# Optimization experiments

Measured on AMD Instinct MI355X. Metric: run time of the kernel, lower is better.

## Reference

```python
import jax, jax.numpy as jnp
import numpy as np

D = 1024
HEADS = 16
HEAD_DIM = D // HEADS
EPS = 1e-5


def layer_norm(x, gamma, beta):
    mu = jnp.mean(x, axis=-1, keepdims=True)
    var = jnp.mean(jnp.square(x - mu), axis=-1, keepdims=True)
    return (x - mu) * jax.lax.rsqrt(var + EPS) * gamma + beta


def setup_inputs() -> dict:
    key = jax.random.key(0)
    ks = jax.random.split(key, 8)
    B, S = 4, 2048
    s_in = 1.0 / np.sqrt(D)
    s_ffn = 1.0 / np.sqrt(4 * D)
    return {
        "x": jax.random.normal(ks[0], (B, S, D), dtype=jnp.float32),
        "ln1_g": jnp.ones((D,), jnp.float32),
        "ln1_b": jnp.zeros((D,), jnp.float32),
        "w_qkv": jax.random.uniform(ks[1], (D, 3 * D), jnp.float32, -s_in, s_in),
        "b_qkv": jnp.zeros((3 * D,), jnp.float32),
        "w_out": jax.random.uniform(ks[2], (D, D), jnp.float32, -s_in, s_in),
        "b_out": jnp.zeros((D,), jnp.float32),
        "ln2_g": jnp.ones((D,), jnp.float32),
        "ln2_b": jnp.zeros((D,), jnp.float32),
        "w_ffn1": jax.random.uniform(ks[3], (D, 4 * D), jnp.float32, -s_in, s_in),
        "b_ffn1": jnp.zeros((4 * D,), jnp.float32),
        "w_ffn2": jax.random.uniform(ks[4], (4 * D, D), jnp.float32, -s_ffn, s_ffn),
        "b_ffn2": jnp.zeros((D,), jnp.float32),
    }


def reference(x, ln1_g, ln1_b, w_qkv, b_qkv, w_out, b_out,
              ln2_g, ln2_b, w_ffn1, b_ffn1, w_ffn2, b_ffn2):
    B, S, Dm = x.shape
    h = layer_norm(x, ln1_g, ln1_b)
    qkv = h @ w_qkv + b_qkv  # [B,S,3D]
    q, k, v = jnp.split(qkv, 3, axis=-1)
    # [B,S,D] -> [B,H,S,hd]
    def to_heads(t):
        return t.reshape(B, S, HEADS, HEAD_DIM).transpose(0, 2, 1, 3)
    q, k, v = to_heads(q), to_heads(k), to_heads(v)
    scores = jnp.einsum('bhqd,bhkd->bhqk', q, k) / np.sqrt(HEAD_DIM).astype(np.float32)
    attn = jax.nn.softmax(scores, axis=-1)
    out = jnp.einsum('bhqk,bhkd->bhqd', attn, v)
    out = out.transpose(0, 2, 1, 3).reshape(B, S, Dm)
    x = x + (out @ w_out + b_out)
    h = layer_norm(x, ln2_g, ln2_b)
    h = jax.nn.gelu(h @ w_ffn1 + b_ffn1, approximate=False) @ w_ffn2 + b_ffn2
    return x + h
```

## Files before the change

### kernel.cpp

```cpp
#include <hip/hip_runtime.h>
#include <cstdint>
#include <cstddef>

typedef unsigned short u16;
typedef unsigned int   u32;
typedef __bf16 bf16x8 __attribute__((ext_vector_type(8)));
typedef float  f32x4  __attribute__((ext_vector_type(4)));
static_assert(sizeof(bf16x8) == 16, "bf16x8 must be 16B");
static_assert(sizeof(f32x4) == 16, "f32x4 must be 16B");

#define DEVI static __device__ __forceinline__

#define QSCALE 0.18033688011112042f

DEVI u16 f2bf(float x) {
  u32 u = __builtin_bit_cast(u32, x);
  u = (u + 0x7FFFu + ((u >> 16) & 1u)) >> 16;
  return (u16)u;
}

DEVI void gload16(const u16* g, u16* l) {
  __builtin_amdgcn_global_load_lds(
      (const __attribute__((address_space(1))) void*)g,
      (__attribute__((address_space(3))) void*)l, 16, 0, 0);
}

#define S_BARRIER() asm volatile("s_barrier" ::: "memory")
#define VMCNT(n) asm volatile("s_waitcnt vmcnt(" #n ")" ::: "memory")

template <int MO, int NACC>
DEVI void mm16(f32x4 (&acc)[NACC][4], const bf16x8 (&af)[4], const bf16x8 (&bf)[4]) {
  __builtin_amdgcn_s_setprio(1);
#pragma unroll
  for (int m = 0; m < 4; m++)
#pragma unroll
    for (int n = 0; n < 4; n++)
      acc[MO + m][n] =
          __builtin_amdgcn_mfma_f32_16x16x32_bf16(af[m], bf[n], acc[MO + m][n], 0, 0, 0);
  __builtin_amdgcn_s_setprio(0);
}

__global__ __launch_bounds__(256) void transpose_cvt(const float* __restrict__ W,
                                                     u16* __restrict__ WT,
                                                     int K, int N,
                                                     float scale, int nscale) {
  __shared__ float tile[32][33];
  int tx = threadIdx.x & 31, ty = threadIdx.x >> 5;
  int c0 = blockIdx.x * 32, r0 = blockIdx.y * 32;
#pragma unroll
  for (int i = 0; i < 4; i++)
    tile[ty + i * 8][tx] = W[(size_t)(r0 + ty + i * 8) * N + c0 + tx];
  __syncthreads();
#pragma unroll
  for (int i = 0; i < 4; i++) {
    int r = ty + i * 8;
    int n = c0 + r;
    float scl = (n < nscale) ? scale : 1.f;
    WT[(size_t)n * K + r0 + tx] = f2bf(tile[tx][r] * scl);
  }
}

__global__ __launch_bounds__(256) void prep_bias(const float* __restrict__ b,
                                                 float* __restrict__ o) {
  int i = blockIdx.x * 256 + threadIdx.x;
  o[i] = b[i] * (i < 1024 ? QSCALE : 1.f);
}

__global__ __launch_bounds__(256) void ln_k(const float* __restrict__ X,
                                            const float* __restrict__ gam,
                                            const float* __restrict__ bet,
                                            u16* __restrict__ H) {
  __shared__ float2 part[4];
  int row = blockIdx.x, t = threadIdx.x;
  const float4* xr = (const float4*)(X + (size_t)row * 1024);
  float4 v = xr[t];
  float s = v.x + v.y + v.z + v.w;
  float q = v.x * v.x + v.y * v.y + v.z * v.z + v.w * v.w;
#pragma unroll
  for (int o = 32; o > 0; o >>= 1) {
    s += __shfl_xor(s, o);
    q += __shfl_xor(q, o);
  }
  if ((t & 63) == 0) part[t >> 6] = make_float2(s, q);
  __syncthreads();
  float S = part[0].x + part[1].x + part[2].x + part[3].x;
  float Q = part[0].y + part[1].y + part[2].y + part[3].y;
  float mu = S * (1.f / 1024.f);
  float rs = rsqrtf(Q * (1.f / 1024.f) - mu * mu + 1e-5f);
  float4 gv = ((const float4*)gam)[t];
  float4 bv = ((const float4*)bet)[t];
  ushort4 o;
  o.x = f2bf((v.x - mu) * rs * gv.x + bv.x);
  o.y = f2bf((v.y - mu) * rs * gv.y + bv.y);
  o.z = f2bf((v.z - mu) * rs * gv.z + bv.z);
  o.w = f2bf((v.w - mu) * rs * gv.w + bv.w);
  *(ushort4*)(H + (size_t)row * 1024 + t * 4) = o;
}

template <int EPI, int NACC>
DEVI void epilogue(f32x4 (&acc)[NACC][4], const float* bias, const float* res,
                   float* outF, u16* outB, int N, int rbase, int cbase, int g, int li) {
#pragma unroll
  for (int n = 0; n < 4; n++) {
    int c = cbase + n * 16 + li;
    float bv = bias[c];
#pragma unroll
    for (int a = 0; a < NACC; a++) {
      int rowb = rbase + a * 16 + g * 4;
#pragma unroll
      for (int r = 0; r < 4; r++) {
        size_t idx = (size_t)(rowb + r) * N + c;
        float v = acc[a][n][r] + bv;
        if constexpr (EPI == 1) {
          v += res[idx];
          outF[idx] = v;
        } else if constexpr (EPI == 2) {
          v = 0.5f * v * (1.f + erff(v * 0.70710678118654752f));
          outB[idx] = f2bf(v);
        } else {
          outB[idx] = f2bf(v);
        }
      }
    }
  }
}

template <int EPI>
__global__ __launch_bounds__(512, 1) void gemm256(const u16* __restrict__ A,
                                                  const u16* __restrict__ Bt,
                                                  const float* __restrict__ bias,
                                                  const float* __restrict__ res,
                                                  float* __restrict__ outF,
                                                  u16* __restrict__ outB,
                                                  int M, int N, int K) {
  __shared__ uint4 As[2][2048];
  __shared__ uint4 Bs[2][2048];
  const int t = threadIdx.x, lane = t & 63, wv = t >> 6;
  const int wr = wv >> 2, wc = wv & 3;
  const int li = lane & 15, g = lane >> 4;

  const int gx = gridDim.x;
  const int nwg = gx * gridDim.y;
  const int wg = blockIdx.y * gx + blockIdx.x;
  const int swz = (wg & 7) * (nwg >> 3) + (wg >> 3);
  const int bx = swz % gx, by = swz / gx;
  const int bm0 = by * 256, bn0 = bx * 256;

  f32x4 acc[8][4];
  const f32x4 z4 = {0.f, 0.f, 0.f, 0.f};
#pragma unroll
  for (int a = 0; a < 8; a++)
#pragma unroll
    for (int n = 0; n < 4; n++) acc[a][n] = z4;

  const u16* aB = A + (size_t)(bm0 + wv * 16 + li) * K + g * 8;
  const u16* bB = Bt + (size_t)(bn0 + wv * 16 + li) * K + g * 8;
  const size_t rskip = (size_t)128 * K;

  auto stA = [&](int buf, int j, int kt) {
    gload16(aB + (size_t)kt * 64 + ((j & 1) ? rskip : (size_t)0) + (j >> 1) * 32,
            (u16*)&As[buf][(j * 8 + wv) * 64]);
  };
  auto stB = [&](int buf, int j, int kt) {
    gload16(bB + (size_t)kt * 64 + ((j & 1) ? rskip : (size_t)0) + (j >> 1) * 32,
            (u16*)&Bs[buf][(j * 8 + wv) * 64]);
  };

  stA(0, 0, 0); stA(0, 1, 0); stB(0, 0, 0); stB(0, 1, 0);
  stA(0, 2, 0); stA(0, 3, 0); stB(0, 2, 0); stB(0, 3, 0);
  VMCNT(4);
  S_BARRIER();

  const int NT = K >> 6;
  int cur = 0;
  for (int kt = 0; kt < NT; kt++) {
    const int nx = cur ^ 1;
    const bool more = (kt + 1 < NT);
    bf16x8 af[4], bf[4];
#pragma unroll
    for (int n = 0; n < 4; n++)
      bf[n] = __builtin_bit_cast(bf16x8, Bs[cur][(wc * 4 + n) * 64 + lane]);
#pragma unroll
    for (int m = 0; m < 4; m++)
      af[m] = __builtin_bit_cast(bf16x8, As[cur][(wr * 8 + m) * 64 + lane]);
    if (more) { stA(nx, 0, kt + 1); stA(nx, 1, kt + 1); }
    S_BARRIER();
    mm16<0>(acc, af, bf);
    S_BARRIER();
#pragma unroll
    for (int m = 0; m < 4; m++)
      af[m] = __builtin_bit_cast(bf16x8, As[cur][(wr * 8 + 4 + m) * 64 + lane]);
    if (more) { stB(nx, 0, kt + 1); stB(nx, 1, kt + 1); }
    S_BARRIER();
    mm16<4>(acc, af, bf);
    if (more) { VMCNT(4); } else { VMCNT(0); }
    S_BARRIER();
#pragma unroll
    for (int n = 0; n < 4; n++)
      bf[n] = __builtin_bit_cast(bf16x8, Bs[cur][(16 + wc * 4 + n) * 64 + lane]);
#pragma unroll
    for (int m = 0; m < 4; m++)
      af[m] = __builtin_bit_cast(bf16x8, As[cur][(16 + wr * 8 + m) * 64 + lane]);
    if (more) { stA(nx, 2, kt + 1); stA(nx, 3, kt + 1); }
    S_BARRIER();
    mm16<0>(acc, af, bf);
    S_BARRIER();
#pragma unroll
    for (int m = 0; m < 4; m++)
      af[m] = __builtin_bit_cast(bf16x8, As[cur][(16 + wr * 8 + 4 + m) * 64 + lane]);
    if (more) { stB(nx, 2, kt + 1); stB(nx, 3, kt + 1); }
    S_BARRIER();
    mm16<4>(acc, af, bf);
    if (more) { VMCNT(4); }
    S_BARRIER();
    cur = nx;
  }

  epilogue<EPI>(acc, bias, res, outF, outB, N, bm0 + wr * 128, bn0 + wc * 64, g, li);
}

template <int EPI>
__global__ __launch_bounds__(512, 1) void gemm128(const u16* __restrict__ A,
                                                  const u16* __restrict__ Bt,
                                                  const float* __restrict__ bias,
                                                  const float* __restrict__ res,
                                                  float* __restrict__ outF,
                                                  u16* __restrict__ outB,
                                                  int M, int N, int K) {
  __shared__ uint4 As[2][1024];
  __shared__ uint4 Bs[2][2048];
  const int t = threadIdx.x, lane = t & 63, wv = t >> 6;
  const int wr = wv >> 2, wc = wv & 3;
  const int li = lane & 15, g = lane >> 4;

  const int gx = gridDim.x;
  const int nwg = gx * gridDim.y;
  const int wg = blockIdx.y * gx + blockIdx.x;
  const int swz = (wg & 7) * (nwg >> 3) + (wg >> 3);
  const int bx = swz % gx, by = swz / gx;
  const int bm0 = by * 128, bn0 = bx * 256;

  f32x4 acc[4][4];
  const f32x4 z4 = {0.f, 0.f, 0.f, 0.f};
#pragma unroll
  for (int a = 0; a < 4; a++)
#pragma unroll
    for (int n = 0; n < 4; n++) acc[a][n] = z4;

  const u16* aB = A + (size_t)(bm0 + wv * 16 + li) * K + g * 8;
  const u16* bB = Bt + (size_t)(bn0 + wv * 16 + li) * K + g * 8;
  const size_t rskip = (size_t)128 * K;

  auto stA = [&](int buf, int j, int kt) {
    gload16(aB + (size_t)kt * 64 + j * 32, (u16*)&As[buf][(j * 8 + wv) * 64]);
  };
  auto stB = [&](int buf, int j, int kt) {
    gload16(bB + (size_t)kt * 64 + ((j & 1) ? rskip : (size_t)0) + (j >> 1) * 32,
            (u16*)&Bs[buf][(j * 8 + wv) * 64]);
  };

  stA(0, 0, 0); stB(0, 0, 0); stB(0, 1, 0);
  stA(0, 1, 0); stB(0, 2, 0); stB(0, 3, 0);
  VMCNT(3);
  S_BARRIER();

  const int NT = K >> 6;
  int cur = 0;
  for (int kt = 0; kt < NT; kt++) {
    const int nx = cur ^ 1;
    const bool more = (kt + 1 < NT);
    bf16x8 af[4], bf[4];
#pragma unroll
    for (int n = 0; n < 4; n++)
      bf[n] = __builtin_bit_cast(bf16x8, Bs[cur][(wc * 4 + n) * 64 + lane]);
#pragma unroll
    for (int m = 0; m < 4; m++)
      af[m] = __builtin_bit_cast(bf16x8, As[cur][(wr * 4 + m) * 64 + lane]);
    if (more) { stA(nx, 0, kt + 1); stB(nx, 0, kt + 1); stB(nx, 1, kt + 1); }
    S_BARRIER();
    mm16<0>(acc, af, bf);
    if (more) { VMCNT(3); } else { VMCNT(0); }
    S_BARRIER();
#pragma unroll
    for (int n = 0; n < 4; n++)
      bf[n] = __builtin_bit_cast(bf16x8, Bs[cur][(16 + wc * 4 + n) * 64 + lane]);
#pragma unroll
    for (int m = 0; m < 4; m++)
      af[m] = __builtin_bit_cast(bf16x8, As[cur][(8 + wr * 4 + m) * 64 + lane]);
    if (more) { stA(nx, 1, kt + 1); stB(nx, 2, kt + 1); stB(nx, 3, kt + 1); }
    S_BARRIER();
    mm16<0>(acc, af, bf);
    if (more) { VMCNT(3); }
    S_BARRIER();
    cur = nx;
  }

  epilogue<EPI>(acc, bias, res, outF, outB, N, bm0 + wr * 64, bn0 + wc * 64, g, li);
}

__global__ __launch_bounds__(256) void v_tr(const u16* __restrict__ qkv,
                                            u16* __restrict__ vfm) {
  __shared__ u16 Vl[64 * 72];
  const int t = threadIdx.x;
  const int bh = blockIdx.y;
  const int bb = bh >> 4, h = bh & 15;
  const int kt = blockIdx.x;
#pragma unroll
  for (int bq = 0; bq < 2; bq++) {
    int c = t + bq * 256;
    int key = c >> 3, d0 = (c & 7) * 8;
    uint4 v = *(const uint4*)(qkv + (size_t)(bb * 2048 + kt * 64 + key) * 3072 + 2048 +
                              h * 64 + d0);
    *(uint4*)&Vl[key * 72 + d0] = v;
  }
  __syncthreads();
#pragma unroll
  for (int bq = 0; bq < 2; bq++) {
    int oc = t + bq * 256;
    int f = oc >> 6, l = oc & 63;
    int db = f >> 1, g32 = f & 1;
    int li = l & 15, g = l >> 4;
    u16 tmp[8];
#pragma unroll
    for (int e = 0; e < 8; e++) {
      int pk = g32 * 32 + ((e & 4) << 2) + g * 4 + (e & 3);
      tmp[e] = Vl[pk * 72 + db * 16 + li];
    }
    *(uint4*)(vfm + ((((size_t)bh * 32 + kt) * 8 + f) * 64 + l) * 8) = *(uint4*)tmp;
  }
}

__global__ __launch_bounds__(256) void attn_k(const u16* __restrict__ qkv,
                                              const u16* __restrict__ vfm,
                                              u16* __restrict__ ao) {
  __shared__ uint4 Ks[512];
  __shared__ uint4 Vs[512];
  const int t = threadIdx.x, lane = t & 63, wv = t >> 6;
  const int g = lane >> 4, li = lane & 15;
  const int bb = blockIdx.y >> 4, h = blockIdx.y & 15;
  const int q0 = blockIdx.x * 64 + wv * 16;

  const size_t qoff = (size_t)(bb * 2048 + q0 + li) * 3072 + h * 64 + g * 8;
  bf16x8 qf0 = __builtin_bit_cast(bf16x8, *(const uint4*)(qkv + qoff));
  bf16x8 qf1 = __builtin_bit_cast(bf16x8, *(const uint4*)(qkv + qoff + 32));

  const u16* kbase = qkv + (size_t)bb * 2048 * 3072 + 1024 + h * 64;
  const int f1 = wv + 4;
  const u16* ksrc0 = kbase + (size_t)(((wv >> 1) << 4) + li) * 3072 + ((wv & 1) << 5) + g * 8;
  const u16* ksrc1 = kbase + (size_t)(((f1 >> 1) << 4) + li) * 3072 + ((f1 & 1) << 5) + g * 8;
  const u16* vsrc0 = vfm + ((size_t)(bb * 16 + h) * 32) * 4096 + (wv * 64 + lane) * 8;
  const u16* vsrc1 = vsrc0 + 4 * 64 * 8;

  const f32x4 z4 = {0.f, 0.f, 0.f, 0.f};
  f32x4 Of[4];
#pragma unroll
  for (int db = 0; db < 4; db++) Of[db] = z4;
  f32x4 Ol = z4;

  bf16x8 vone;
#pragma unroll
  for (int j = 0; j < 8; j++) vone[j] = (__bf16)1.0f;

  for (int tile = 0; tile < 32; tile++) {
    __syncthreads();
    gload16(ksrc0 + (size_t)tile * 64 * 3072, (u16*)&Ks[wv * 64]);
    gload16(ksrc1 + (size_t)tile * 64 * 3072, (u16*)&Ks[(wv + 4) * 64]);
    gload16(vsrc0 + (size_t)tile * 4096, (u16*)&Vs[wv * 64]);
    gload16(vsrc1 + (size_t)tile * 4096, (u16*)&Vs[(wv + 4) * 64]);
    __syncthreads();

#pragma unroll
    for (int g32 = 0; g32 < 2; g32++) {
      bf16x8 pf;
#pragma unroll
      for (int tt = 0; tt < 2; tt++) {
        int kb16 = g32 * 2 + tt;
        bf16x8 k0f = __builtin_bit_cast(bf16x8, Ks[(kb16 * 2 + 0) * 64 + lane]);
        bf16x8 k1f = __builtin_bit_cast(bf16x8, Ks[(kb16 * 2 + 1) * 64 + lane]);
        f32x4 st = z4;
        st = __builtin_amdgcn_mfma_f32_16x16x32_bf16(k0f, qf0, st, 0, 0, 0);
        st = __builtin_amdgcn_mfma_f32_16x16x32_bf16(k1f, qf1, st, 0, 0, 0);
#pragma unroll
        for (int r = 0; r < 4; r++) pf[tt * 4 + r] = (__bf16)exp2f(st[r]);
      }
      __builtin_amdgcn_s_setprio(1);
#pragma unroll
      for (int db = 0; db < 4; db++) {
        bf16x8 vf = __builtin_bit_cast(bf16x8, Vs[(db * 2 + g32) * 64 + lane]);
        Of[db] = __builtin_amdgcn_mfma_f32_16x16x32_bf16(pf, vf, Of[db], 0, 0, 0);
      }
      Ol = __builtin_amdgcn_mfma_f32_16x16x32_bf16(pf, vone, Ol, 0, 0, 0);
      __builtin_amdgcn_s_setprio(0);
    }
  }

  float invl[4];
#pragma unroll
  for (int r = 0; r < 4; r++) invl[r] = 1.f / Ol[r];
#pragma unroll
  for (int db = 0; db < 4; db++)
#pragma unroll
    for (int r = 0; r < 4; r++)
      ao[(size_t)(bb * 2048 + q0 + 4 * g + r) * 1024 + h * 64 + db * 16 + li] =
          f2bf(Of[db][r] * invl[r]);
}

extern "C" void kernel_launch(void* const* d_in, const int* in_sizes, int n_in,
                              void* d_out, int out_size, void* d_ws, size_t ws_size,
                              hipStream_t stream) {
  const float* x = (const float*)d_in[0];
  const float* ln1g = (const float*)d_in[1];
  const float* ln1b = (const float*)d_in[2];
  const float* wqkv = (const float*)d_in[3];
  const float* bqkv = (const float*)d_in[4];
  const float* wout = (const float*)d_in[5];
  const float* bout = (const float*)d_in[6];
  const float* ln2g = (const float*)d_in[7];
  const float* ln2b = (const float*)d_in[8];
  const float* wff1 = (const float*)d_in[9];
  const float* bff1 = (const float*)d_in[10];
  const float* wff2 = (const float*)d_in[11];
  const float* bff2 = (const float*)d_in[12];
  float* outF = (float*)d_out;
  char* ws = (char*)d_ws;

  u16* wqkvT = (u16*)(ws + 0);
  u16* woutT = (u16*)(ws + 6291456);
  u16* wff1T = (u16*)(ws + 8388608);
  u16* wff2T = (u16*)(ws + 16777216);
  u16* hbuf  = (u16*)(ws + 25165824);
  u16* vfm   = (u16*)(ws + 25165824);
  u16* qkvb  = (u16*)(ws + 41943040);
  u16* attnb = (u16*)(ws + 92274688);
  u16* ffn1b = qkvb;
  float* biasq = (float*)attnb;

  transpose_cvt<<<dim3(96, 32), 256, 0, stream>>>(wqkv, wqkvT, 1024, 3072, QSCALE, 1024);
  transpose_cvt<<<dim3(32, 32), 256, 0, stream>>>(wout, woutT, 1024, 1024, 1.f, 0);
  transpose_cvt<<<dim3(128, 32), 256, 0, stream>>>(wff1, wff1T, 1024, 4096, 1.f, 0);
  transpose_cvt<<<dim3(32, 128), 256, 0, stream>>>(wff2, wff2T, 4096, 1024, 1.f, 0);
  prep_bias<<<12, 256, 0, stream>>>(bqkv, biasq);

  ln_k<<<8192, 256, 0, stream>>>(x, ln1g, ln1b, hbuf);
  gemm256<0><<<dim3(12, 32), 512, 0, stream>>>(hbuf, wqkvT, biasq, nullptr, nullptr, qkvb,
                                               8192, 3072, 1024);
  v_tr<<<dim3(32, 64), 256, 0, stream>>>(qkvb, vfm);
  attn_k<<<dim3(32, 64), 256, 0, stream>>>(qkvb, vfm, attnb);
  gemm128<1><<<dim3(4, 64), 512, 0, stream>>>(attnb, woutT, bout, x, outF, nullptr,
                                              8192, 1024, 1024);
  ln_k<<<8192, 256, 0, stream>>>(outF, ln2g, ln2b, hbuf);
  gemm256<2><<<dim3(16, 32), 512, 0, stream>>>(hbuf, wff1T, bff1, nullptr, nullptr, ffn1b,
                                               8192, 4096, 1024);
  gemm128<1><<<dim3(4, 64), 512, 0, stream>>>(ffn1b, wff2T, bff2, outF, outF, nullptr,
                                              8192, 1024, 4096);

  (void)in_sizes;
  (void)n_in;
  (void)out_size;
  (void)ws_size;
}
```

Before: 487.3 us.

## Use 4-stage half-K-tile LDS pipeline in GEMMs and 128-row tiles for QKV

```diff
diff --git a/kernel.cpp b/kernel.cpp
--- a/kernel.cpp
+++ b/kernel.cpp
@@ -133,8 +133,8 @@
                                                   float* __restrict__ outF,
                                                   u16* __restrict__ outB,
                                                   int M, int N, int K) {
-  __shared__ uint4 As[2][2048];
-  __shared__ uint4 Bs[2][2048];
+  __shared__ uint4 As[4][1024];
+  __shared__ uint4 Bs[4][1024];
   const int t = threadIdx.x, lane = t & 63, wv = t >> 6;
   const int wr = wv >> 2, wc = wv & 3;
   const int li = lane & 15, g = lane >> 4;
@@ -153,67 +153,46 @@
 #pragma unroll
     for (int n = 0; n < 4; n++) acc[a][n] = z4;
 
-  const u16* aB = A + (size_t)(bm0 + wv * 16 + li) * K + g * 8;
-  const u16* bB = Bt + (size_t)(bn0 + wv * 16 + li) * K + g * 8;
-  const size_t rskip = (size_t)128 * K;
-
-  auto stA = [&](int buf, int j, int kt) {
-    gload16(aB + (size_t)kt * 64 + ((j & 1) ? rskip : (size_t)0) + (j >> 1) * 32,
-            (u16*)&As[buf][(j * 8 + wv) * 64]);
+  const u16* aB = A + (size_t)(bm0 + wv * 32 + li) * K + g * 8;
+  const u16* bB = Bt + (size_t)(bn0 + wv * 32 + li) * K + g * 8;
+  const size_t fstep = (size_t)16 * K;
+
+  auto stage = [&](int hh) {
+    const int s = hh & 3;
+    const size_t ko = (size_t)(hh >> 1) * 64 + (size_t)(hh & 1) * 32;
+    gload16(aB + ko, (u16*)&As[s][(2 * wv + 0) * 64]);
+    gload16(aB + fstep + ko, (u16*)&As[s][(2 * wv + 1) * 64]);
+    gload16(bB + ko, (u16*)&Bs[s][(2 * wv + 0) * 64]);
+    gload16(bB + fstep + ko, (u16*)&Bs[s][(2 * wv + 1) * 64]);
   };
-  auto stB = [&](int buf, int j, int kt) {
-    gload16(bB + (size_t)kt * 64 + ((j & 1) ? rskip : (size_t)0) + (j >> 1) * 32,
-            (u16*)&Bs[buf][(j * 8 + wv) * 64]);
-  };
-
-  stA(0, 0, 0); stA(0, 1, 0); stB(0, 0, 0); stB(0, 1, 0);
-  stA(0, 2, 0); stA(0, 3, 0); stB(0, 2, 0); stB(0, 3, 0);
-  VMCNT(4);
+
+  const int NH = K >> 5;
+  stage(0); stage(1); stage(2);
+  VMCNT(8);
   S_BARRIER();
 
-  const int NT = K >> 6;
-  int cur = 0;
-  for (int kt = 0; kt < NT; kt++) {
-    const int nx = cur ^ 1;
-    const bool more = (kt + 1 < NT);
+  for (int hh = 0; hh < NH; hh++) {
+    const int s = hh & 3;
     bf16x8 af[4], bf[4];
 #pragma unroll
     for (int n = 0; n < 4; n++)
-      bf[n] = __builtin_bit_cast(bf16x8, Bs[cur][(wc * 4 + n) * 64 + lane]);
+      bf[n] = __builtin_bit_cast(bf16x8, Bs[s][(wc * 4 + n) * 64 + lane]);
 #pragma unroll
     for (int m = 0; m < 4; m++)
-      af[m] = __builtin_bit_cast(bf16x8, As[cur][(wr * 8 + m) * 64 + lane]);
-    if (more) { stA(nx, 0, kt + 1); stA(nx, 1, kt + 1); }
+      af[m] = __builtin_bit_cast(bf16x8, As[s][(wr * 8 + m) * 64 + lane]);
+    if (hh + 3 < NH) stage(hh + 3);
     S_BARRIER();
     mm16<0>(acc, af, bf);
     S_BARRIER();
 #pragma unroll
     for (int m = 0; m < 4; m++)
-      af[m] = __builtin_bit_cast(bf16x8, As[cur][(wr * 8 + 4 + m) * 64 + lane]);
-    if (more) { stB(nx, 0, kt + 1); stB(nx, 1, kt + 1); }
+      af[m] = __builtin_bit_cast(bf16x8, As[s][(wr * 8 + 4 + m) * 64 + lane]);
     S_BARRIER();
     mm16<4>(acc, af, bf);
-    if (more) { VMCNT(4); } else { VMCNT(0); }
-    S_BARRIER();
-#pragma unroll
-    for (int n = 0; n < 4; n++)
-      bf[n] = __builtin_bit_cast(bf16x8, Bs[cur][(16 + wc * 4 + n) * 64 + lane]);
-#pragma unroll
-    for (int m = 0; m < 4; m++)
-      af[m] = __builtin_bit_cast(bf16x8, As[cur][(16 + wr * 8 + m) * 64 + lane]);
-    if (more) { stA(nx, 2, kt + 1); stA(nx, 3, kt + 1); }
-    S_BARRIER();
-    mm16<0>(acc, af, bf);
-    S_BARRIER();
-#pragma unroll
-    for (int m = 0; m < 4; m++)
-      af[m] = __builtin_bit_cast(bf16x8, As[cur][(16 + wr * 8 + 4 + m) * 64 + lane]);
-    if (more) { stB(nx, 2, kt + 1); stB(nx, 3, kt + 1); }
-    S_BARRIER();
-    mm16<4>(acc, af, bf);
-    if (more) { VMCNT(4); }
-    S_BARRIER();
-    cur = nx;
+    if (hh + 3 < NH) { VMCNT(8); }
+    else if (hh + 2 < NH) { VMCNT(4); }
+    else if (hh + 1 < NH) { VMCNT(0); }
+    S_BARRIER();
   }
 
   epilogue<EPI>(acc, bias, res, outF, outB, N, bm0 + wr * 128, bn0 + wc * 64, g, li);
@@ -227,8 +206,8 @@
                                                   float* __restrict__ outF,
                                                   u16* __restrict__ outB,
                                                   int M, int N, int K) {
-  __shared__ uint4 As[2][1024];
-  __shared__ uint4 Bs[2][2048];
+  __shared__ uint4 As[4][512];
+  __shared__ uint4 Bs[4][1024];
   const int t = threadIdx.x, lane = t & 63, wv = t >> 6;
   const int wr = wv >> 2, wc = wv & 3;
   const int li = lane & 15, g = lane >> 4;
@@ -248,51 +227,38 @@
     for (int n = 0; n < 4; n++) acc[a][n] = z4;
 
   const u16* aB = A + (size_t)(bm0 + wv * 16 + li) * K + g * 8;
-  const u16* bB = Bt + (size_t)(bn0 + wv * 16 + li) * K + g * 8;
-  const size_t rskip = (size_t)128 * K;
-
-  auto stA = [&](int buf, int j, int kt) {
-    gload16(aB + (size_t)kt * 64 + j * 32, (u16*)&As[buf][(j * 8 + wv) * 64]);
+  const u16* bB = Bt + (size_t)(bn0 + wv * 32 + li) * K + g * 8;
+  const size_t fstep = (size_t)16 * K;
+
+  auto stage = [&](int hh) {
+    const int s = hh & 3;
+    const size_t ko = (size_t)(hh >> 1) * 64 + (size_t)(hh & 1) * 32;
+    gload16(aB + ko, (u16*)&As[s][wv * 64]);
+    gload16(bB + ko, (u16*)&Bs[s][(2 * wv + 0) * 64]);
+    gload16(bB + fstep + ko, (u16*)&Bs[s][(2 * wv + 1) * 64]);
   };
-  auto stB = [&](int buf, int j, int kt) {
-    gload16(bB + (size_t)kt * 64 + ((j & 1) ? rskip : (size_t)0) + (j >> 1) * 32,
-            (u16*)&Bs[buf][(j * 8 + wv) * 64]);
-  };
-
-  stA(0, 0, 0); stB(0, 0, 0); stB(0, 1, 0);
-  stA(0, 1, 0); stB(0, 2, 0); stB(0, 3, 0);
-  VMCNT(3);
+
+  const int NH = K >> 5;
+  stage(0); stage(1); stage(2);
+  VMCNT(6);
   S_BARRIER();
 
-  const int NT = K >> 6;
-  int cur = 0;
-  for (int kt = 0; kt < NT; kt++) {
-    const int nx = cur ^ 1;
-    const bool more = (kt + 1 < NT);
+  for (int hh = 0; hh < NH; hh++) {
+    const int s = hh & 3;
     bf16x8 af[4], bf[4];
 #pragma unroll
     for (int n = 0; n < 4; n++)
-      bf[n] = __builtin_bit_cast(bf16x8, Bs[cur][(wc * 4 + n) * 64 + lane]);
+      bf[n] = __builtin_bit_cast(bf16x8, Bs[s][(wc * 4 + n) * 64 + lane]);
 #pragma unroll
     for (int m = 0; m < 4; m++)
-      af[m] = __builtin_bit_cast(bf16x8, As[cur][(wr * 4 + m) * 64 + lane]);
-    if (more) { stA(nx, 0, kt + 1); stB(nx, 0, kt + 1); stB(nx, 1, kt + 1); }
+      af[m] = __builtin_bit_cast(bf16x8, As[s][(wr * 4 + m) * 64 + lane]);
+    if (hh + 3 < NH) stage(hh + 3);
     S_BARRIER();
     mm16<0>(acc, af, bf);
-    if (more) { VMCNT(3); } else { VMCNT(0); }
-    S_BARRIER();
-#pragma unroll
-    for (int n = 0; n < 4; n++)
-      bf[n] = __builtin_bit_cast(bf16x8, Bs[cur][(16 + wc * 4 + n) * 64 + lane]);
-#pragma unroll
-    for (int m = 0; m < 4; m++)
-      af[m] = __builtin_bit_cast(bf16x8, As[cur][(8 + wr * 4 + m) * 64 + lane]);
-    if (more) { stA(nx, 1, kt + 1); stB(nx, 2, kt + 1); stB(nx, 3, kt + 1); }
-    S_BARRIER();
-    mm16<0>(acc, af, bf);
-    if (more) { VMCNT(3); }
-    S_BARRIER();
-    cur = nx;
+    if (hh + 3 < NH) { VMCNT(6); }
+    else if (hh + 2 < NH) { VMCNT(3); }
+    else if (hh + 1 < NH) { VMCNT(0); }
+    S_BARRIER();
   }
 
   epilogue<EPI>(acc, bias, res, outF, outB, N, bm0 + wr * 64, bn0 + wc * 64, g, li);
@@ -442,7 +408,7 @@
   prep_bias<<<12, 256, 0, stream>>>(bqkv, biasq);
 
   ln_k<<<8192, 256, 0, stream>>>(x, ln1g, ln1b, hbuf);
-  gemm256<0><<<dim3(12, 32), 512, 0, stream>>>(hbuf, wqkvT, biasq, nullptr, nullptr, qkvb,
+  gemm128<0><<<dim3(12, 64), 512, 0, stream>>>(hbuf, wqkvT, biasq, nullptr, nullptr, qkvb,
                                                8192, 3072, 1024);
   v_tr<<<dim3(32, 64), 256, 0, stream>>>(qkvb, vfm);
   attn_k<<<dim3(32, 64), 256, 0, stream>>>(qkvb, vfm, attnb);
```

Measured after the change: 505.1 us. +3.7%, slower.

## Run FFN1 GEMM with 1024 threads and move QKV GEMM to 128-row tiles

Applied to the files above, without the earlier changes.

```diff
diff --git a/kernel.cpp b/kernel.cpp
--- a/kernel.cpp
+++ b/kernel.cpp
@@ -126,13 +126,13 @@
 }
 
 template <int EPI>
-__global__ __launch_bounds__(512, 1) void gemm256(const u16* __restrict__ A,
-                                                  const u16* __restrict__ Bt,
-                                                  const float* __restrict__ bias,
-                                                  const float* __restrict__ res,
-                                                  float* __restrict__ outF,
-                                                  u16* __restrict__ outB,
-                                                  int M, int N, int K) {
+__global__ __launch_bounds__(1024, 4) void gemm256(const u16* __restrict__ A,
+                                                   const u16* __restrict__ Bt,
+                                                   const float* __restrict__ bias,
+                                                   const float* __restrict__ res,
+                                                   float* __restrict__ outF,
+                                                   u16* __restrict__ outB,
+                                                   int M, int N, int K) {
   __shared__ uint4 As[2][2048];
   __shared__ uint4 Bs[2][2048];
   const int t = threadIdx.x, lane = t & 63, wv = t >> 6;
@@ -146,29 +146,26 @@
   const int bx = swz % gx, by = swz / gx;
   const int bm0 = by * 256, bn0 = bx * 256;
 
-  f32x4 acc[8][4];
+  f32x4 acc[4][4];
   const f32x4 z4 = {0.f, 0.f, 0.f, 0.f};
 #pragma unroll
-  for (int a = 0; a < 8; a++)
+  for (int a = 0; a < 4; a++)
 #pragma unroll
     for (int n = 0; n < 4; n++) acc[a][n] = z4;
 
   const u16* aB = A + (size_t)(bm0 + wv * 16 + li) * K + g * 8;
   const u16* bB = Bt + (size_t)(bn0 + wv * 16 + li) * K + g * 8;
-  const size_t rskip = (size_t)128 * K;
-
-  auto stA = [&](int buf, int j, int kt) {
-    gload16(aB + (size_t)kt * 64 + ((j & 1) ? rskip : (size_t)0) + (j >> 1) * 32,
-            (u16*)&As[buf][(j * 8 + wv) * 64]);
+
+  auto stA = [&](int buf, int kh, int kt) {
+    gload16(aB + (size_t)kt * 64 + kh * 32, (u16*)&As[buf][(kh * 16 + wv) * 64]);
   };
-  auto stB = [&](int buf, int j, int kt) {
-    gload16(bB + (size_t)kt * 64 + ((j & 1) ? rskip : (size_t)0) + (j >> 1) * 32,
-            (u16*)&Bs[buf][(j * 8 + wv) * 64]);
+  auto stB = [&](int buf, int kh, int kt) {
+    gload16(bB + (size_t)kt * 64 + kh * 32, (u16*)&Bs[buf][(kh * 16 + wv) * 64]);
   };
 
-  stA(0, 0, 0); stA(0, 1, 0); stB(0, 0, 0); stB(0, 1, 0);
-  stA(0, 2, 0); stA(0, 3, 0); stB(0, 2, 0); stB(0, 3, 0);
-  VMCNT(4);
+  stA(0, 0, 0); stB(0, 0, 0);
+  stA(0, 1, 0); stB(0, 1, 0);
+  VMCNT(2);
   S_BARRIER();
 
   const int NT = K >> 6;
@@ -182,41 +179,27 @@
       bf[n] = __builtin_bit_cast(bf16x8, Bs[cur][(wc * 4 + n) * 64 + lane]);
 #pragma unroll
     for (int m = 0; m < 4; m++)
-      af[m] = __builtin_bit_cast(bf16x8, As[cur][(wr * 8 + m) * 64 + lane]);
-    if (more) { stA(nx, 0, kt + 1); stA(nx, 1, kt + 1); }
+      af[m] = __builtin_bit_cast(bf16x8, As[cur][(wr * 4 + m) * 64 + lane]);
+    if (more) { stA(nx, 0, kt + 1); stB(nx, 0, kt + 1); }
     S_BARRIER();
     mm16<0>(acc, af, bf);
-    S_BARRIER();
-#pragma unroll
-    for (int m = 0; m < 4; m++)
-      af[m] = __builtin_bit_cast(bf16x8, As[cur][(wr * 8 + 4 + m) * 64 + lane]);
-    if (more) { stB(nx, 0, kt + 1); stB(nx, 1, kt + 1); }
-    S_BARRIER();
-    mm16<4>(acc, af, bf);
-    if (more) { VMCNT(4); } else { VMCNT(0); }
+    if (more) { VMCNT(2); } else { VMCNT(0); }
     S_BARRIER();
 #pragma unroll
     for (int n = 0; n < 4; n++)
       bf[n] = __builtin_bit_cast(bf16x8, Bs[cur][(16 + wc * 4 + n) * 64 + lane]);
 #pragma unroll
     for (int m = 0; m < 4; m++)
-      af[m] = __builtin_bit_cast(bf16x8, As[cur][(16 + wr * 8 + m) * 64 + lane]);
-    if (more) { stA(nx, 2, kt + 1); stA(nx, 3, kt + 1); }
+      af[m] = __builtin_bit_cast(bf16x8, As[cur][(16 + wr * 4 + m) * 64 + lane]);
+    if (more) { stA(nx, 1, kt + 1); stB(nx, 1, kt + 1); }
     S_BARRIER();
     mm16<0>(acc, af, bf);
-    S_BARRIER();
-#pragma unroll
-    for (int m = 0; m < 4; m++)
-      af[m] = __builtin_bit_cast(bf16x8, As[cur][(16 + wr * 8 + 4 + m) * 64 + lane]);
-    if (more) { stB(nx, 2, kt + 1); stB(nx, 3, kt + 1); }
-    S_BARRIER();
-    mm16<4>(acc, af, bf);
-    if (more) { VMCNT(4); }
+    if (more) { VMCNT(2); }
     S_BARRIER();
     cur = nx;
   }
 
-  epilogue<EPI>(acc, bias, res, outF, outB, N, bm0 + wr * 128, bn0 + wc * 64, g, li);
+  epilogue<EPI>(acc, bias, res, outF, outB, N, bm0 + wr * 64, bn0 + wc * 64, g, li);
 }
 
 template <int EPI>
@@ -442,15 +425,15 @@
   prep_bias<<<12, 256, 0, stream>>>(bqkv, biasq);
 
   ln_k<<<8192, 256, 0, stream>>>(x, ln1g, ln1b, hbuf);
-  gemm256<0><<<dim3(12, 32), 512, 0, stream>>>(hbuf, wqkvT, biasq, nullptr, nullptr, qkvb,
+  gemm128<0><<<dim3(12, 64), 512, 0, stream>>>(hbuf, wqkvT, biasq, nullptr, nullptr, qkvb,
                                                8192, 3072, 1024);
   v_tr<<<dim3(32, 64), 256, 0, stream>>>(qkvb, vfm);
   attn_k<<<dim3(32, 64), 256, 0, stream>>>(qkvb, vfm, attnb);
   gemm128<1><<<dim3(4, 64), 512, 0, stream>>>(attnb, woutT, bout, x, outF, nullptr,
                                               8192, 1024, 1024);
   ln_k<<<8192, 256, 0, stream>>>(outF, ln2g, ln2b, hbuf);
-  gemm256<2><<<dim3(16, 32), 512, 0, stream>>>(hbuf, wff1T, bff1, nullptr, nullptr, ffn1b,
-                                               8192, 4096, 1024);
+  gemm256<2><<<dim3(16, 32), 1024, 0, stream>>>(hbuf, wff1T, bff1, nullptr, nullptr, ffn1b,
+                                                8192, 4096, 1024);
   gemm128<1><<<dim3(4, 64), 512, 0, stream>>>(ffn1b, wff2T, bff2, outF, outF, nullptr,
                                               8192, 1024, 4096);
 
```

After: 477.0 us. -2.1%, faster.
